# Kernel tuning notes

Hardware: AMD Instinct MI355X
Metric: run time of the kernel (lower is better)

Reference implementation:

```python
import jax, jax.numpy as jnp
import numpy as np

NEG_INF = -1e9
ROUTING_ITERS = 3


def squash(z):
    # z: [B, K, D]
    norm_sq = jnp.sum(z * z, axis=-1, keepdims=True)
    norm = jnp.sqrt(norm_sq + 1e-8)
    return norm_sq / (1.0 + norm_sq) * (z / norm)


def setup_inputs() -> dict:
    key = jax.random.key(0)
    k1, k2, k3, k4 = jax.random.split(key, 4)
    B, L, D, K = 2048, 200, 256, 8
    behavior_embeds = jax.random.normal(k1, (B, L, D), dtype=jnp.float32)
    W = jax.random.normal(k2, (D, D), dtype=jnp.float32) * (1.0 / np.sqrt(D))
    b_init = jax.random.normal(k3, (B, K, L), dtype=jnp.float32)
    mask = jax.random.randint(k4, (B, L), 0, 2, dtype=jnp.int32)
    return {"behavior_embeds": behavior_embeds, "W": W, "b_init": b_init, "mask": mask}


def reference(behavior_embeds, W, b_init, mask):
    # behavior_embeds: [B, L, D]; W: [D, D] (nn.Linear weight, y = x @ W.T)
    u_hat = jnp.einsum('bld,ed->ble', behavior_embeds, W)  # [B, L, D]
    # mask padding positions in routing logits
    b = jnp.where(mask[:, None, :] == 0, NEG_INF, b_init)  # [B, K, L]
    c = None
    for i in range(ROUTING_ITERS):
        w = jax.nn.softmax(b, axis=2)                      # [B, K, L]
        z = jnp.einsum('bkl,bld->bkd', w, u_hat)           # [B, K, D]
        c = squash(z)
        if i < ROUTING_ITERS - 1:
            b = b + jnp.einsum('bkd,bld->bkl', c, u_hat)
    return c
```

## Files before the change

### kernel.cpp

```cpp
#include <hip/hip_runtime.h>
#include <hip/hip_bf16.h>

#define B_ 2048
#define L_ 200
#define D_ 256
#define K_ 8

typedef __attribute__((ext_vector_type(8))) _Float16 half8;
typedef __attribute__((ext_vector_type(4))) _Float16 half4v;
typedef __attribute__((ext_vector_type(4))) float f32x4;

#define LTP 232
#define WP  232
#define CP  264

#define OFF_UTT  0
#define OFF_WH   118784
#define OFF_WL   126208
#define OFF_XA   133632
#define OFF_XB   142080
#define OFF_LB   150528
#define OFF_RED  156928
#define OFF_SC   157440
#define LDS_TOTAL 157472

__global__ __launch_bounds__(256) void w_to_f16(const float* __restrict__ W,
                                                _Float16* __restrict__ Wh) {
    const int idx = (blockIdx.x * 256 + threadIdx.x) * 4;
    const float4 v = *(const float4*)(W + idx);
    half4v h = { (_Float16)v.x, (_Float16)v.y, (_Float16)v.z, (_Float16)v.w };
    *(half4v*)(Wh + idx) = h;
}

__global__ __launch_bounds__(1024) void fused_mie2(
        const float* __restrict__ X, const float* __restrict__ b_init,
        const int* __restrict__ mask, const _Float16* __restrict__ Wh,
        float* __restrict__ out) {
    extern __shared__ char dyn[];
    _Float16* utT = (_Float16*)(dyn + OFF_UTT);
    _Float16* wHs = (_Float16*)(dyn + OFF_WH);
    _Float16* wLs = (_Float16*)(dyn + OFF_WL);
    _Float16* XsA = (_Float16*)(dyn + OFF_XA);
    _Float16* XsB = (_Float16*)(dyn + OFF_XB);
    _Float16* cHs = (_Float16*)(dyn + OFF_XA);
    _Float16* cLs = (_Float16*)(dyn + OFF_XB);
    float* lb   = (float*)(dyn + OFF_LB);
    float* red2 = (float*)(dyn + OFF_RED);
    float* scS  = (float*)(dyn + OFF_SC);

    const int b = blockIdx.x;
    const int t = threadIdx.x;
    const int w = t >> 6, lane = t & 63;
    const int fr = lane & 15, hi = lane >> 4;

    {
        const int row = t >> 2, part = t & 3;
        *(int4*)&utT[row * LTP + 200 + 8 * part] = make_int4(0, 0, 0, 0);
    }
    if (t < 928) *(int4*)(dyn + OFF_WH + 16 * t) = make_int4(0, 0, 0, 0);
    for (int idx = t; idx < K_ * L_; idx += 1024) {
        const int k = idx / L_, l = idx - k * L_;
        lb[idx] = (mask[b * L_ + l] == 0) ? -1e9f
                                          : b_init[(size_t)b * (K_ * L_) + idx];
    }

    half8 bw[8];
    {
        const _Float16* wr = Wh + (size_t)(16 * w + fr) * 256;
#pragma unroll
        for (int d0 = 0; d0 < 8; ++d0)
            bw[d0] = *(const half8*)(wr + 32 * d0 + 8 * hi);
    }

    const float* Xb = X + (size_t)b * L_ * D_;
    const int sc4 = lane * 4;
    {
        const float4 v = *(const float4*)(Xb + w * 256 + sc4);
        half4v h = { (_Float16)v.x, (_Float16)v.y, (_Float16)v.z, (_Float16)v.w };
        *(half4v*)&XsA[w * CP + sc4] = h;
    }
    __syncthreads();

    for (int lt = 0; lt < 13; ++lt) {
        _Float16* cur = (lt & 1) ? XsB : XsA;
        _Float16* nxt = (lt & 1) ? XsA : XsB;
        float4 xv = make_float4(0.f, 0.f, 0.f, 0.f);
        if (lt < 12) {
            const int l = 16 * (lt + 1) + w;
            if (l < L_) xv = *(const float4*)(Xb + l * 256 + sc4);
        }
        f32x4 acc = {};
#pragma unroll
        for (int d0 = 0; d0 < 8; ++d0) {
            const half8 a8 = *(const half8*)&cur[fr * CP + 32 * d0 + 8 * hi];
            acc = __builtin_amdgcn_mfma_f32_16x16x32_f16(bw[d0], a8, acc, 0, 0, 0);
        }
#pragma unroll
        for (int j = 0; j < 4; ++j)
            utT[(16 * w + 4 * hi + j) * LTP + 16 * lt + fr] = (_Float16)acc[j];
        if (lt < 12) {
            half4v h = { (_Float16)xv.x, (_Float16)xv.y, (_Float16)xv.z, (_Float16)xv.w };
            *(half4v*)&nxt[w * CP + sc4] = h;
        }
        __syncthreads();
    }

    half8 au[8];
    if (w < 13) {
#pragma unroll
        for (int d0 = 0; d0 < 8; ++d0) {
            _Float16 tmp[8];
#pragma unroll
            for (int j = 0; j < 8; ++j)
                tmp[j] = utT[(32 * d0 + 8 * hi + j) * LTP + 16 * w + fr];
            au[d0] = *(half8*)tmp;
        }
    }

    for (int iter = 0; iter < 3; ++iter) {
        if (t < 512) {
            const int k = t >> 6, ln = t & 63;
            float v[4];
            float m = -1e30f;
#pragma unroll
            for (int i = 0; i < 4; ++i) {
                const int l = ln + 64 * i;
                v[i] = (l < L_) ? lb[k * L_ + l] : -1e30f;
                m = fmaxf(m, v[i]);
            }
#pragma unroll
            for (int off = 32; off >= 1; off >>= 1)
                m = fmaxf(m, __shfl_xor(m, off));
            float e[4], s = 0.f;
#pragma unroll
            for (int i = 0; i < 4; ++i) {
                const int l = ln + 64 * i;
                e[i] = (l < L_) ? __expf(v[i] - m) : 0.f;
                s += e[i];
            }
#pragma unroll
            for (int off = 32; off >= 1; off >>= 1)
                s += __shfl_xor(s, off);
            const float rinv = 1.0f / s;
#pragma unroll
            for (int i = 0; i < 4; ++i) {
                const int l = ln + 64 * i;
                if (l < L_) {
                    const float wv = e[i] * rinv;
                    const _Float16 h = (_Float16)wv;
                    wHs[k * WP + l] = h;
                    wLs[k * WP + l] = (_Float16)(wv - (float)h);
                }
            }
        }
        __syncthreads();

        f32x4 zac = {};
#pragma unroll
        for (int ks = 0; ks < 7; ++ks) {
            const half8 bz = *(const half8*)&utT[(16 * w + fr) * LTP + 32 * ks + 8 * hi];
            const half8 ah = *(const half8*)&wHs[fr * WP + 32 * ks + 8 * hi];
            const half8 al = *(const half8*)&wLs[fr * WP + 32 * ks + 8 * hi];
            zac = __builtin_amdgcn_mfma_f32_16x16x32_f16(ah, bz, zac, 0, 0, 0);
            zac = __builtin_amdgcn_mfma_f32_16x16x32_f16(al, bz, zac, 0, 0, 0);
        }

        float sq0 = zac[0] * zac[0], sq1 = zac[1] * zac[1];
        float sq2 = zac[2] * zac[2], sq3 = zac[3] * zac[3];
#pragma unroll
        for (int off = 1; off <= 8; off <<= 1) {
            sq0 += __shfl_xor(sq0, off);
            sq1 += __shfl_xor(sq1, off);
            sq2 += __shfl_xor(sq2, off);
            sq3 += __shfl_xor(sq3, off);
        }
        if (fr == 0 && hi < 2) {
            f32x4 sv = { sq0, sq1, sq2, sq3 };
            *(f32x4*)&red2[w * 8 + 4 * hi] = sv;
        }
        __syncthreads();
        if (t < 8) {
            float ns = 0.f;
#pragma unroll
            for (int ww = 0; ww < 16; ++ww) ns += red2[ww * 8 + t];
            scS[t] = ns / ((1.f + ns) * sqrtf(ns + 1e-8f));
        }
        __syncthreads();

        if (iter == 2) {
            if (hi < 2) {
                const f32x4 sc = *(const f32x4*)&scS[4 * hi];
                float* op = out + (size_t)b * (K_ * D_) + (4 * hi) * D_ + 16 * w + fr;
#pragma unroll
                for (int j = 0; j < 4; ++j) op[j * D_] = sc[j] * zac[j];
            }
        } else {
            if (hi < 2) {
                const f32x4 sc = *(const f32x4*)&scS[4 * hi];
#pragma unroll
                for (int j = 0; j < 4; ++j) {
                    const float v = sc[j] * zac[j];
                    const _Float16 h = (_Float16)v;
                    cHs[(4 * hi + j) * CP + 16 * w + fr] = h;
                    cLs[(4 * hi + j) * CP + 16 * w + fr] = (_Float16)(v - (float)h);
                }
            }
            __syncthreads();

            if (w < 13) {
                f32x4 dac = {};
#pragma unroll
                for (int d0 = 0; d0 < 8; ++d0) {
                    const half8 bh = *(const half8*)&cHs[fr * CP + 32 * d0 + 8 * hi];
                    const half8 bl = *(const half8*)&cLs[fr * CP + 32 * d0 + 8 * hi];
                    dac = __builtin_amdgcn_mfma_f32_16x16x32_f16(au[d0], bh, dac, 0, 0, 0);
                    dac = __builtin_amdgcn_mfma_f32_16x16x32_f16(au[d0], bl, dac, 0, 0, 0);
                }
                if (fr < 8) {
#pragma unroll
                    for (int j = 0; j < 4; ++j) {
                        const int l = 16 * w + 4 * hi + j;
                        if (l < L_) lb[fr * L_ + l] += dac[j];
                    }
                }
            }
            __syncthreads();
        }
    }
}

extern "C" void kernel_launch(void* const* d_in, const int* in_sizes, int n_in,
                              void* d_out, int out_size, void* d_ws, size_t ws_size,
                              hipStream_t stream) {
    (void)in_sizes; (void)n_in; (void)out_size; (void)ws_size;
    const float* behavior = (const float*)d_in[0];
    const float* W        = (const float*)d_in[1];
    const float* b_init   = (const float*)d_in[2];
    const int*   mask     = (const int*)d_in[3];
    float* out      = (float*)d_out;
    _Float16* Wh    = (_Float16*)d_ws;

    hipFuncSetAttribute((const void*)fused_mie2,
                        hipFuncAttributeMaxDynamicSharedMemorySize, LDS_TOTAL);

    w_to_f16<<<64, 256, 0, stream>>>(W, Wh);
    fused_mie2<<<B_, 1024, LDS_TOTAL, stream>>>(behavior, b_init, mask, Wh, out);
}
```

Before: 264.8 us.

## Keep projected u_hat in registers to shrink LDS and raise occupancy

Replaces the full u_hat tile in shared memory (~119KB) with two small double-buffered 16-column staging tiles. Each projection step is redistributed straight into per-thread register fragments (zf for the z-reduction, au for the logit update). This cuts LDS from ~157KB to ~63KB, so more workgroups can be resident per CU (launch bounds request 4), and it splits MFMA accumulators into independent chains to shorten dependency stalls. It also replaces the scale broadcast through shared memory plus a barrier with wave shuffles. The risk is heavy register pressure at 1024 threads with 4 blocks requested, which could cause spills.

```diff
diff --git a/kernel.cpp b/kernel.cpp
--- a/kernel.cpp
+++ b/kernel.cpp
@@ -10,19 +10,19 @@
 typedef __attribute__((ext_vector_type(4))) _Float16 half4v;
 typedef __attribute__((ext_vector_type(4))) float f32x4;
 
-#define LTP 232
-#define WP  232
-#define CP  264
-
-#define OFF_UTT  0
-#define OFF_WH   118784
-#define OFF_WL   126208
-#define OFF_XA   133632
-#define OFF_XB   142080
-#define OFF_LB   150528
-#define OFF_RED  156928
-#define OFF_SC   157440
-#define LDS_TOTAL 157472
+#define USTP 24
+#define WP   232
+#define CP   264
+
+#define OFF_UST0 0
+#define OFF_UST1 12288
+#define OFF_WH   24576
+#define OFF_WL   32000
+#define OFF_CH   39424
+#define OFF_CL   47872
+#define OFF_LB   56320
+#define OFF_RED  62720
+#define LDS_TOTAL 63232
 
 __global__ __launch_bounds__(256) void w_to_f16(const float* __restrict__ W,
                                                 _Float16* __restrict__ Wh) {
@@ -32,31 +32,27 @@
     *(half4v*)(Wh + idx) = h;
 }
 
-__global__ __launch_bounds__(1024) void fused_mie2(
+__global__ __launch_bounds__(1024, 4) void fused_mie3(
         const float* __restrict__ X, const float* __restrict__ b_init,
         const int* __restrict__ mask, const _Float16* __restrict__ Wh,
         float* __restrict__ out) {
     extern __shared__ char dyn[];
-    _Float16* utT = (_Float16*)(dyn + OFF_UTT);
-    _Float16* wHs = (_Float16*)(dyn + OFF_WH);
-    _Float16* wLs = (_Float16*)(dyn + OFF_WL);
-    _Float16* XsA = (_Float16*)(dyn + OFF_XA);
-    _Float16* XsB = (_Float16*)(dyn + OFF_XB);
-    _Float16* cHs = (_Float16*)(dyn + OFF_XA);
-    _Float16* cLs = (_Float16*)(dyn + OFF_XB);
+    _Float16* UsT0 = (_Float16*)(dyn + OFF_UST0);
+    _Float16* UsT1 = (_Float16*)(dyn + OFF_UST1);
+    _Float16* wHs  = (_Float16*)(dyn + OFF_WH);
+    _Float16* wLs  = (_Float16*)(dyn + OFF_WL);
+    _Float16* cHs  = (_Float16*)(dyn + OFF_CH);
+    _Float16* cLs  = (_Float16*)(dyn + OFF_CL);
+    _Float16* XsA  = (_Float16*)(dyn + OFF_CH);
+    _Float16* XsB  = (_Float16*)(dyn + OFF_CL);
     float* lb   = (float*)(dyn + OFF_LB);
     float* red2 = (float*)(dyn + OFF_RED);
-    float* scS  = (float*)(dyn + OFF_SC);
 
     const int b = blockIdx.x;
     const int t = threadIdx.x;
     const int w = t >> 6, lane = t & 63;
     const int fr = lane & 15, hi = lane >> 4;
 
-    {
-        const int row = t >> 2, part = t & 3;
-        *(int4*)&utT[row * LTP + 200 + 8 * part] = make_int4(0, 0, 0, 0);
-    }
     if (t < 928) *(int4*)(dyn + OFF_WH + 16 * t) = make_int4(0, 0, 0, 0);
     for (int idx = t; idx < K_ * L_; idx += 1024) {
         const int k = idx / L_, l = idx - k * L_;
@@ -81,39 +77,74 @@
     }
     __syncthreads();
 
+    half8 zf[7];
+    zf[6] = (half8){ (_Float16)0, (_Float16)0, (_Float16)0, (_Float16)0,
+                     (_Float16)0, (_Float16)0, (_Float16)0, (_Float16)0 };
+    half8 au[8];
+
+#pragma unroll
     for (int lt = 0; lt < 13; ++lt) {
-        _Float16* cur = (lt & 1) ? XsB : XsA;
-        _Float16* nxt = (lt & 1) ? XsA : XsB;
+        _Float16* xcur = (lt & 1) ? XsB : XsA;
+        _Float16* xnxt = (lt & 1) ? XsA : XsB;
+        _Float16* ucur = (lt & 1) ? UsT1 : UsT0;
+        _Float16* uprv = (lt & 1) ? UsT0 : UsT1;
+
         float4 xv = make_float4(0.f, 0.f, 0.f, 0.f);
         if (lt < 12) {
             const int l = 16 * (lt + 1) + w;
             if (l < L_) xv = *(const float4*)(Xb + l * 256 + sc4);
         }
-        f32x4 acc = {};
-#pragma unroll
-        for (int d0 = 0; d0 < 8; ++d0) {
-            const half8 a8 = *(const half8*)&cur[fr * CP + 32 * d0 + 8 * hi];
-            acc = __builtin_amdgcn_mfma_f32_16x16x32_f16(bw[d0], a8, acc, 0, 0, 0);
-        }
+
+        f32x4 a1 = {}, a2 = {};
+#pragma unroll
+        for (int d0 = 0; d0 < 4; ++d0) {
+            const half8 x8 = *(const half8*)&xcur[fr * CP + 32 * d0 + 8 * hi];
+            a1 = __builtin_amdgcn_mfma_f32_16x16x32_f16(bw[d0], x8, a1, 0, 0, 0);
+        }
+#pragma unroll
+        for (int d0 = 4; d0 < 8; ++d0) {
+            const half8 x8 = *(const half8*)&xcur[fr * CP + 32 * d0 + 8 * hi];
+            a2 = __builtin_amdgcn_mfma_f32_16x16x32_f16(bw[d0], x8, a2, 0, 0, 0);
+        }
+
+        if (lt > 0) {
+            const int pt = lt - 1;
+            if ((hi >> 1) == (pt & 1))
+                zf[pt >> 1] = *(const half8*)&uprv[(16 * w + fr) * USTP + 8 * (hi & 1)];
+            if (w == pt) {
+#pragma unroll
+                for (int d0 = 0; d0 < 8; ++d0) {
+                    _Float16 tmp[8];
+#pragma unroll
+                    for (int j = 0; j < 8; ++j)
+                        tmp[j] = uprv[(32 * d0 + 8 * hi + j) * USTP + fr];
+                    au[d0] = *(half8*)tmp;
+                }
+            }
+        }
+
 #pragma unroll
         for (int j = 0; j < 4; ++j)
-            utT[(16 * w + 4 * hi + j) * LTP + 16 * lt + fr] = (_Float16)acc[j];
+            ucur[(16 * w + 4 * hi + j) * USTP + fr] = (_Float16)(a1[j] + a2[j]);
+
         if (lt < 12) {
             half4v h = { (_Float16)xv.x, (_Float16)xv.y, (_Float16)xv.z, (_Float16)xv.w };
-            *(half4v*)&nxt[w * CP + sc4] = h;
+            *(half4v*)&xnxt[w * CP + sc4] = h;
         }
         __syncthreads();
     }
-
-    half8 au[8];
-    if (w < 13) {
-#pragma unroll
-        for (int d0 = 0; d0 < 8; ++d0) {
-            _Float16 tmp[8];
-#pragma unroll
-            for (int j = 0; j < 8; ++j)
-                tmp[j] = utT[(32 * d0 + 8 * hi + j) * LTP + 16 * w + fr];
-            au[d0] = *(half8*)tmp;
+    {
+        if ((hi >> 1) == 0)
+            zf[6] = *(const half8*)&UsT0[(16 * w + fr) * USTP + 8 * (hi & 1)];
+        if (w == 12) {
+#pragma unroll
+            for (int d0 = 0; d0 < 8; ++d0) {
+                _Float16 tmp[8];
+#pragma unroll
+                for (int j = 0; j < 8; ++j)
+                    tmp[j] = UsT0[(32 * d0 + 8 * hi + j) * USTP + fr];
+                au[d0] = *(half8*)tmp;
+            }
         }
     }
 
@@ -155,18 +186,18 @@
         }
         __syncthreads();
 
-        f32x4 zac = {};
+        f32x4 zH = {}, zL = {};
 #pragma unroll
         for (int ks = 0; ks < 7; ++ks) {
-            const half8 bz = *(const half8*)&utT[(16 * w + fr) * LTP + 32 * ks + 8 * hi];
             const half8 ah = *(const half8*)&wHs[fr * WP + 32 * ks + 8 * hi];
             const half8 al = *(const half8*)&wLs[fr * WP + 32 * ks + 8 * hi];
-            zac = __builtin_amdgcn_mfma_f32_16x16x32_f16(ah, bz, zac, 0, 0, 0);
-            zac = __builtin_amdgcn_mfma_f32_16x16x32_f16(al, bz, zac, 0, 0, 0);
-        }
-
-        float sq0 = zac[0] * zac[0], sq1 = zac[1] * zac[1];
-        float sq2 = zac[2] * zac[2], sq3 = zac[3] * zac[3];
+            zH = __builtin_amdgcn_mfma_f32_16x16x32_f16(ah, zf[ks], zH, 0, 0, 0);
+            zL = __builtin_amdgcn_mfma_f32_16x16x32_f16(al, zf[ks], zL, 0, 0, 0);
+        }
+        const float z0 = zH[0] + zL[0], z1 = zH[1] + zL[1];
+        const float z2 = zH[2] + zL[2], z3 = zH[3] + zL[3];
+
+        float sq0 = z0 * z0, sq1 = z1 * z1, sq2 = z2 * z2, sq3 = z3 * z3;
 #pragma unroll
         for (int off = 1; off <= 8; off <<= 1) {
             sq0 += __shfl_xor(sq0, off);
@@ -179,48 +210,59 @@
             *(f32x4*)&red2[w * 8 + 4 * hi] = sv;
         }
         __syncthreads();
-        if (t < 8) {
+
+        float myscale = 0.f;
+        if (lane < 8) {
             float ns = 0.f;
 #pragma unroll
-            for (int ww = 0; ww < 16; ++ww) ns += red2[ww * 8 + t];
-            scS[t] = ns / ((1.f + ns) * sqrtf(ns + 1e-8f));
-        }
-        __syncthreads();
+            for (int ww = 0; ww < 16; ++ww) ns += red2[ww * 8 + lane];
+            myscale = ns / ((1.f + ns) * sqrtf(ns + 1e-8f));
+        }
+        const float sc0 = __shfl(myscale, 4 * hi + 0);
+        const float sc1 = __shfl(myscale, 4 * hi + 1);
+        const float sc2 = __shfl(myscale, 4 * hi + 2);
+        const float sc3 = __shfl(myscale, 4 * hi + 3);
 
         if (iter == 2) {
             if (hi < 2) {
-                const f32x4 sc = *(const f32x4*)&scS[4 * hi];
                 float* op = out + (size_t)b * (K_ * D_) + (4 * hi) * D_ + 16 * w + fr;
-#pragma unroll
-                for (int j = 0; j < 4; ++j) op[j * D_] = sc[j] * zac[j];
+                op[0 * D_] = sc0 * z0;
+                op[1 * D_] = sc1 * z1;
+                op[2 * D_] = sc2 * z2;
+                op[3 * D_] = sc3 * z3;
             }
         } else {
             if (hi < 2) {
-                const f32x4 sc = *(const f32x4*)&scS[4 * hi];
-#pragma unroll
-                for (int j = 0; j < 4; ++j) {
-                    const float v = sc[j] * zac[j];
-                    const _Float16 h = (_Float16)v;
-                    cHs[(4 * hi + j) * CP + 16 * w + fr] = h;
-                    cLs[(4 * hi + j) * CP + 16 * w + fr] = (_Float16)(v - (float)h);
-                }
+                const float v0 = sc0 * z0, v1 = sc1 * z1;
+                const float v2 = sc2 * z2, v3 = sc3 * z3;
+                const _Float16 h0 = (_Float16)v0, h1 = (_Float16)v1;
+                const _Float16 h2 = (_Float16)v2, h3 = (_Float16)v3;
+                const int cb = 16 * w + fr;
+                cHs[(4 * hi + 0) * CP + cb] = h0;
+                cHs[(4 * hi + 1) * CP + cb] = h1;
+                cHs[(4 * hi + 2) * CP + cb] = h2;
+                cHs[(4 * hi + 3) * CP + cb] = h3;
+                cLs[(4 * hi + 0) * CP + cb] = (_Float16)(v0 - (float)h0);
+                cLs[(4 * hi + 1) * CP + cb] = (_Float16)(v1 - (float)h1);
+                cLs[(4 * hi + 2) * CP + cb] = (_Float16)(v2 - (float)h2);
+                cLs[(4 * hi + 3) * CP + cb] = (_Float16)(v3 - (float)h3);
             }
             __syncthreads();
 
             if (w < 13) {
-                f32x4 dac = {};
+                f32x4 dH = {}, dL = {};
 #pragma unroll
                 for (int d0 = 0; d0 < 8; ++d0) {
                     const half8 bh = *(const half8*)&cHs[fr * CP + 32 * d0 + 8 * hi];
                     const half8 bl = *(const half8*)&cLs[fr * CP + 32 * d0 + 8 * hi];
-                    dac = __builtin_amdgcn_mfma_f32_16x16x32_f16(au[d0], bh, dac, 0, 0, 0);
-                    dac = __builtin_amdgcn_mfma_f32_16x16x32_f16(au[d0], bl, dac, 0, 0, 0);
+                    dH = __builtin_amdgcn_mfma_f32_16x16x32_f16(au[d0], bh, dH, 0, 0, 0);
+                    dL = __builtin_amdgcn_mfma_f32_16x16x32_f16(au[d0], bl, dL, 0, 0, 0);
                 }
                 if (fr < 8) {
 #pragma unroll
                     for (int j = 0; j < 4; ++j) {
                         const int l = 16 * w + 4 * hi + j;
-                        if (l < L_) lb[fr * L_ + l] += dac[j];
+                        if (l < L_) lb[fr * L_ + l] += dH[j] + dL[j];
                     }
                 }
             }
@@ -240,9 +282,9 @@
     float* out      = (float*)d_out;
     _Float16* Wh    = (_Float16*)d_ws;
 
-    hipFuncSetAttribute((const void*)fused_mie2,
+    hipFuncSetAttribute((const void*)fused_mie3,
                         hipFuncAttributeMaxDynamicSharedMemorySize, LDS_TOTAL);
 
     w_to_f16<<<64, 256, 0, stream>>>(W, Wh);
-    fused_mie2<<<B_, 1024, LDS_TOTAL, stream>>>(behavior, b_init, mask, Wh, out);
+    fused_mie3<<<B_, 1024, LDS_TOTAL, stream>>>(behavior, b_init, mask, Wh, out);
 }
```

Measured after the change: 345.5 us. 30.5% more time.
